# Kernel tuning notes

Hardware: AMD Instinct MI355X
Metric: run time of the kernel (lower is better)

## Reference

```python
import jax, jax.numpy as jnp
import numpy as np

K = 4  # number of neighbors, per kNN-VC convention

def setup_inputs() -> dict:
    key = jax.random.key(0)
    k1, k2 = jax.random.split(key)
    source_feats = jax.random.normal(k1, (2048, 1024), dtype=jnp.float32)
    target_feats = jax.random.normal(k2, (50000, 1024), dtype=jnp.float32)
    return {"source_feats": source_feats, "target_feats": target_feats}

def reference(source_feats, target_feats):
    # cosine kNN matching: for each source frame, find K nearest target frames
    # under cosine distance (= highest cosine similarity), then average them.
    eps = jnp.asarray(1e-8, source_feats.dtype)
    src_n = source_feats / jnp.maximum(jnp.linalg.norm(source_feats, axis=-1, keepdims=True), eps)
    tgt_n = target_feats / jnp.maximum(jnp.linalg.norm(target_feats, axis=-1, keepdims=True), eps)
    # [T_src, T_tgt] cosine similarity
    sims = jnp.einsum('sd,td->st', src_n, tgt_n)
    _, idx = jax.lax.top_k(sims, K)          # [T_src, K]
    neighbors = target_feats[idx]             # [T_src, K, D]
    out = jnp.mean(neighbors, axis=1)         # [T_src, D]
    return out
```

## Files before the change

### kernel.cpp

```cpp
#include <hip/hip_runtime.h>
#include <math.h>

#define S_ROWS 2048
#define T_ROWS 50000
#define DIM    1024
#define KNN    4

#define BM 128
#define BN 128
#define KSL 64
#define NSLAB (DIM / KSL)
#define NBUF 3
#define TILES_PER_CHUNK 2
#define CHUNK_COLS (BN * TILES_PER_CHUNK)
#define NUM_CHUNKS ((T_ROWS + CHUNK_COLS - 1) / CHUNK_COLS)
#define T_PAD (NUM_CHUNKS * CHUNK_COLS)
#define NCAND (NUM_CHUNKS * KNN)
#define REFINE 16
#define SP 67
#define QSCALE 500.0f

typedef unsigned int uint;
typedef unsigned long long u64;
typedef signed char i8;
typedef __attribute__((ext_vector_type(4))) int i32x4;

__device__ __forceinline__ u64 packI(int v, int idx) {
  return ((u64)((uint)v ^ 0x80000000u) << 32) | (uint)(~idx);
}

template <int N>
__device__ __forceinline__ void insU(u64 p, u64 (&tv)[N]) {
  if (p <= tv[N - 1]) return;
  tv[N - 1] = p;
#pragma unroll
  for (int j = N - 1; j > 0; --j) {
    if (tv[j] > tv[j - 1]) { u64 t = tv[j]; tv[j] = tv[j - 1]; tv[j - 1] = t; }
  }
}

__device__ __forceinline__ void llds16(const void* g, void* l) {
  __builtin_amdgcn_global_load_lds(
      reinterpret_cast<__attribute__((address_space(1))) void*>(
          reinterpret_cast<uintptr_t>(g)),
      reinterpret_cast<__attribute__((address_space(3))) void*>(
          (unsigned)reinterpret_cast<uintptr_t>(l)),
      16, 0, 0);
}

__device__ __forceinline__ int imax2(int a, int b) { return a > b ? a : b; }

__global__ __launch_bounds__(256) void quant2_kernel(const float* __restrict__ srcf,
                                                     const float* __restrict__ tgtf,
                                                     i8* __restrict__ srcq,
                                                     i8* __restrict__ tgtq) {
  const int b = blockIdx.x;
  const int tid = threadIdx.x;
  const bool isT = b < T_PAD;
  const int row = isT ? b : b - T_PAD;
  const float* in = isT ? tgtf : srcf;
  i8* outq = isT ? tgtq : srcq;
  const int nvalid = isT ? T_ROWS : S_ROWS;
  if (row >= nvalid) {
    ((uint*)(outq + ((size_t)row << 10)))[tid] = 0u;
    return;
  }
  __shared__ float red[4];
  float4 v = ((const float4*)(in + ((size_t)row << 10)))[tid];
  float s = v.x * v.x + v.y * v.y + v.z * v.z + v.w * v.w;
#pragma unroll
  for (int off = 32; off; off >>= 1) s += __shfl_down(s, off, 64);
  if ((tid & 63) == 0) red[tid >> 6] = s;
  __syncthreads();
  float tot = red[0] + red[1] + red[2] + red[3];
  float r = QSCALE / fmaxf(sqrtf(tot), 1e-8f);
  int q0 = __float2int_rn(v.x * r), q1 = __float2int_rn(v.y * r);
  int q2 = __float2int_rn(v.z * r), q3 = __float2int_rn(v.w * r);
  q0 = imax2(-127, (q0 < 127 ? q0 : 127));
  q1 = imax2(-127, (q1 < 127 ? q1 : 127));
  q2 = imax2(-127, (q2 < 127 ? q2 : 127));
  q3 = imax2(-127, (q3 < 127 ? q3 : 127));
  uint packed = ((uint)q0 & 255u) | (((uint)q1 & 255u) << 8) |
                (((uint)q2 & 255u) << 16) | (((uint)q3 & 255u) << 24);
  ((uint*)(outq + ((size_t)row << 10)))[tid] = packed;
}

union __align__(16) SimSmem {
  i8 ab[NBUF][2 * BM * KSL];
  int sims[BM * SP];
  u64 mb[256 * KNN];
};

__device__ __forceinline__ void stage64(const i8* aP, const i8* bP, i8* aL, i8* bL) {
  llds16(aP, aL);
  llds16(aP + 16384, aL + 1024);
  llds16(bP, bL);
  llds16(bP + 16384, bL + 1024);
}

__global__ __launch_bounds__(256, 3) void sim_i8_kernel(const i8* __restrict__ srcq,
                                                        const i8* __restrict__ tgtq,
                                                        u64* __restrict__ partials) {
  __shared__ SimSmem sm;

  const int tid = threadIdx.x;
  const int lane = tid & 63;
  const int wave = tid >> 6;
  const int qr = (wave >> 1) * 64;
  const int qch = wave & 1;
  const int m = lane & 15;
  const int quad = lane >> 4;
  const int r0 = blockIdx.x * BM;
  const int chunk = blockIdx.y;

  const int srow4 = lane >> 2;
  const int scb4 = (lane & 3) ^ (srow4 & 3);
  const i8* aLane = srcq + (((size_t)(r0 + wave * 32 + srow4)) << 10) + scb4 * 16;

  const int swz = (quad ^ (m & 3)) << 4;
  const int aoff0 = ((qr + m) << 6) + swz;
  const int boff0 = ((qch * 64 + m) << 6) + swz;

  u64 topp[KNN] = {0, 0, 0, 0};
  int thrI = (int)0x80000000;

  for (int tile = 0; tile < TILES_PER_CHUNK; ++tile) {
    const int c0 = chunk * CHUNK_COLS + tile * BN;
    const i8* bLane = tgtq + (((size_t)(c0 + wave * 32 + srow4)) << 10) + scb4 * 16;

    i32x4 acc[4][4];
#pragma unroll
    for (int i = 0; i < 4; ++i)
#pragma unroll
      for (int j = 0; j < 4; ++j) acc[i][j] = (i32x4){0, 0, 0, 0};

    stage64(aLane, bLane, sm.ab[0] + wave * 2048, sm.ab[0] + 8192 + wave * 2048);
    stage64(aLane + 64, bLane + 64, sm.ab[1] + wave * 2048, sm.ab[1] + 8192 + wave * 2048);

#pragma unroll
    for (int k = 0; k < NSLAB; ++k) {
      if (k == NSLAB - 1)
        asm volatile("s_waitcnt vmcnt(0)" ::: "memory");
      else
        asm volatile("s_waitcnt vmcnt(4)" ::: "memory");
      asm volatile("s_waitcnt lgkmcnt(0)" ::: "memory");
      __builtin_amdgcn_s_barrier();
      __builtin_amdgcn_sched_barrier(0);

      const i8* base = sm.ab[k % NBUF];
      i32x4 af[4], bf[4];
#pragma unroll
      for (int i = 0; i < 4; ++i) af[i] = *(const i32x4*)(base + aoff0 + i * 1024);
#pragma unroll
      for (int j = 0; j < 4; ++j) bf[j] = *(const i32x4*)(base + 8192 + boff0 + j * 1024);

      if (k + 2 < NSLAB) {
        i8* nb = sm.ab[(k + 2) % NBUF];
        stage64(aLane + ((k + 2) << 6), bLane + ((k + 2) << 6),
                nb + wave * 2048, nb + 8192 + wave * 2048);
      }

      __builtin_amdgcn_s_setprio(1);
#pragma unroll
      for (int i = 0; i < 4; ++i)
#pragma unroll
        for (int j = 0; j < 4; ++j)
          acc[i][j] = __builtin_amdgcn_mfma_i32_16x16x64_i8(af[i], bf[j], acc[i][j], 0, 0, 0);
      __builtin_amdgcn_s_setprio(0);
    }

    __syncthreads();

#pragma unroll
    for (int ph = 0; ph < 2; ++ph) {
      if (qch == ph) {
#pragma unroll
        for (int i = 0; i < 4; ++i)
#pragma unroll
          for (int j = 0; j < 4; ++j)
#pragma unroll
            for (int reg = 0; reg < 4; ++reg)
              sm.sims[(qr + i * 16 + quad * 4 + reg) * SP + j * 16 + m] = acc[i][j][reg];
      }
      __syncthreads();
      {
        const int rowl = tid & 127;
        const int chh = tid >> 7;
        const int* srow = &sm.sims[rowl * SP + chh * 32];
        const int gbase = c0 + ph * 64 + chh * 32;
#pragma unroll
        for (int c = 0; c < 32; c += 4) {
          int a = srow[c], b = srow[c + 1], d2 = srow[c + 2], e = srow[c + 3];
          int mx = imax2(imax2(a, b), imax2(d2, e));
          if (mx > thrI) {
            const int g = gbase + c;
            if (g + 0 < T_ROWS) insU<KNN>(packI(a, g + 0), topp);
            if (g + 1 < T_ROWS) insU<KNN>(packI(b, g + 1), topp);
            if (g + 2 < T_ROWS) insU<KNN>(packI(d2, g + 2), topp);
            if (g + 3 < T_ROWS) insU<KNN>(packI(e, g + 3), topp);
            thrI = (int)((uint)(topp[KNN - 1] >> 32) ^ 0x80000000u);
          }
        }
      }
      __syncthreads();
    }
  }

#pragma unroll
  for (int j = 0; j < KNN; ++j) sm.mb[tid * KNN + j] = topp[j];
  __syncthreads();
  if (tid < 128) {
#pragma unroll
    for (int j = 0; j < KNN; ++j) insU<KNN>(sm.mb[(tid + 128) * KNN + j], topp);
    u64* dst = partials + ((size_t)(r0 + tid) * NUM_CHUNKS + chunk) * KNN;
#pragma unroll
    for (int j = 0; j < KNN; ++j) dst[j] = topp[j];
  }
}

__global__ __launch_bounds__(256) void merge_gather_kernel(
    const u64* __restrict__ partials, const float* __restrict__ src,
    const float* __restrict__ tgt, float* __restrict__ out) {
  const int row = blockIdx.x;
  const int tid = threadIdx.x;
  const int lane = tid & 63;
  const int wave = tid >> 6;
  __shared__ u64 cbuf[NCAND];
  __shared__ u64 part8[8][REFINE];
  __shared__ int cand[REFINE];
  __shared__ double cval[REFINE];
  __shared__ int fin[KNN];

  for (int c = tid; c < NCAND; c += 256) cbuf[c] = partials[(size_t)row * NCAND + c];
  __syncthreads();

  if (tid < 8) {
    u64 t16[REFINE];
#pragma unroll
    for (int j = 0; j < REFINE; ++j) t16[j] = 0;
    const int base = tid * (NCAND / 8);
    for (int c = 0; c < NCAND / 8; ++c) insU<REFINE>(cbuf[base + c], t16);
#pragma unroll
    for (int j = 0; j < REFINE; ++j) part8[tid][j] = t16[j];
  }
  __syncthreads();
  if (tid == 0) {
    u64 t16[REFINE];
#pragma unroll
    for (int j = 0; j < REFINE; ++j) t16[j] = 0;
    for (int s = 0; s < 8; ++s)
#pragma unroll
      for (int j = 0; j < REFINE; ++j) insU<REFINE>(part8[s][j], t16);
#pragma unroll
    for (int j = 0; j < REFINE; ++j) cand[j] = (int)(~(uint)t16[j]);
  }
  __syncthreads();

  const float4* s4 = (const float4*)(src + ((size_t)row << 10));
  float4 s0 = s4[lane], s1 = s4[lane + 64], s2 = s4[lane + 128], s3 = s4[lane + 192];
  double ss = (double)s0.x * s0.x + (double)s0.y * s0.y + (double)s0.z * s0.z + (double)s0.w * s0.w
            + (double)s1.x * s1.x + (double)s1.y * s1.y + (double)s1.z * s1.z + (double)s1.w * s1.w
            + (double)s2.x * s2.x + (double)s2.y * s2.y + (double)s2.z * s2.z + (double)s2.w * s2.w
            + (double)s3.x * s3.x + (double)s3.y * s3.y + (double)s3.z * s3.z + (double)s3.w * s3.w;
#pragma unroll
  for (int off = 32; off; off >>= 1) ss += __shfl_down(ss, off, 64);
  ss = __shfl(ss, 0, 64);
  const double sn = fmax(sqrt(ss), 1e-8);

  for (int cc = wave; cc < REFINE; cc += 4) {
    const float4* t4 = (const float4*)(tgt + ((size_t)cand[cc] << 10));
    float4 t0 = t4[lane], t1 = t4[lane + 64], t2 = t4[lane + 128], t3 = t4[lane + 192];
    double dd = (double)s0.x * t0.x + (double)s0.y * t0.y + (double)s0.z * t0.z + (double)s0.w * t0.w
              + (double)s1.x * t1.x + (double)s1.y * t1.y + (double)s1.z * t1.z + (double)s1.w * t1.w
              + (double)s2.x * t2.x + (double)s2.y * t2.y + (double)s2.z * t2.z + (double)s2.w * t2.w
              + (double)s3.x * t3.x + (double)s3.y * t3.y + (double)s3.z * t3.z + (double)s3.w * t3.w;
    double tt = (double)t0.x * t0.x + (double)t0.y * t0.y + (double)t0.z * t0.z + (double)t0.w * t0.w
              + (double)t1.x * t1.x + (double)t1.y * t1.y + (double)t1.z * t1.z + (double)t1.w * t1.w
              + (double)t2.x * t2.x + (double)t2.y * t2.y + (double)t2.z * t2.z + (double)t2.w * t2.w
              + (double)t3.x * t3.x + (double)t3.y * t3.y + (double)t3.z * t3.z + (double)t3.w * t3.w;
#pragma unroll
    for (int off = 32; off; off >>= 1) {
      dd += __shfl_down(dd, off, 64);
      tt += __shfl_down(tt, off, 64);
    }
    if (lane == 0) cval[cc] = dd / (sn * fmax(sqrt(tt), 1e-8));
  }
  __syncthreads();

  if (tid == 0) {
    bool used[REFINE];
#pragma unroll
    for (int j = 0; j < REFINE; ++j) used[j] = false;
    for (int k = 0; k < KNN; ++k) {
      int bj = -1; double bv = 0.0; int bidx = 0x7fffffff;
      for (int j = 0; j < REFINE; ++j) {
        if (used[j]) continue;
        if (bj < 0 || cval[j] > bv || (cval[j] == bv && cand[j] < bidx)) {
          bj = j; bv = cval[j]; bidx = cand[j];
        }
      }
      used[bj] = true;
      fin[k] = cand[bj];
    }
  }
  __syncthreads();

  const int d = tid * 4;
  float4 a = *(const float4*)(tgt + ((size_t)fin[0] << 10) + d);
  float4 b = *(const float4*)(tgt + ((size_t)fin[1] << 10) + d);
  float4 c = *(const float4*)(tgt + ((size_t)fin[2] << 10) + d);
  float4 e = *(const float4*)(tgt + ((size_t)fin[3] << 10) + d);
  float4 o;
  o.x = 0.25f * (a.x + b.x + c.x + e.x);
  o.y = 0.25f * (a.y + b.y + c.y + e.y);
  o.z = 0.25f * (a.z + b.z + c.z + e.z);
  o.w = 0.25f * (a.w + b.w + c.w + e.w);
  *(float4*)(out + ((size_t)row << 10) + d) = o;
}

extern "C" void kernel_launch(void* const* d_in, const int* in_sizes, int n_in,
                              void* d_out, int out_size, void* d_ws, size_t ws_size,
                              hipStream_t stream) {
  const float* src = (const float*)d_in[0];
  const float* tgt = (const float*)d_in[1];
  float* out = (float*)d_out;
  char* ws = (char*)d_ws;

  const size_t SRCQ_B = (size_t)S_ROWS << 10;
  const size_t TGTQ_B = (size_t)T_PAD << 10;

  i8* srcq = (i8*)ws;
  i8* tgtq = (i8*)(ws + SRCQ_B);
  u64* partials = (u64*)(ws + SRCQ_B + TGTQ_B);

  quant2_kernel<<<T_PAD + S_ROWS, 256, 0, stream>>>(src, tgt, srcq, tgtq);

  dim3 g3(S_ROWS / BM, NUM_CHUNKS);
  sim_i8_kernel<<<g3, 256, 0, stream>>>(srcq, tgtq, partials);

  merge_gather_kernel<<<S_ROWS, 256, 0, stream>>>(partials, src, tgt, out);
}
```

Baseline: 681.5 us.

## Restructure similarity kernel into single-wave 64x64 blocks without barriers

Replaces the 256-thread 128x128 block with a single-wavefront block covering 64 source rows and four 64-column tiles per chunk. Double buffering uses a two-stage LDS ring, and with only one wave per block all workgroup barriers and the cross-wave top-k merge are removed. Each lane owns one source row and does its top-4 selection directly. The cost is less data reuse per block, with each wave loading A and B tiles alone, and more blocks. Occupancy depends on how many 64-thread blocks fit per CU given the LDS use.

```diff
diff --git a/kernel.cpp b/kernel.cpp
--- a/kernel.cpp
+++ b/kernel.cpp
@@ -6,13 +6,13 @@
 #define DIM    1024
 #define KNN    4
 
-#define BM 128
-#define BN 128
+#define BM 64
+#define TN 64
+#define TILES 4
 #define KSL 64
 #define NSLAB (DIM / KSL)
-#define NBUF 3
-#define TILES_PER_CHUNK 2
-#define CHUNK_COLS (BN * TILES_PER_CHUNK)
+#define NBUF 2
+#define CHUNK_COLS (TN * TILES)
 #define NUM_CHUNKS ((T_ROWS + CHUNK_COLS - 1) / CHUNK_COLS)
 #define T_PAD (NUM_CHUNKS * CHUNK_COLS)
 #define NCAND (NUM_CHUNKS * KNN)
@@ -88,45 +88,46 @@
 union __align__(16) SimSmem {
   i8 ab[NBUF][2 * BM * KSL];
   int sims[BM * SP];
-  u64 mb[256 * KNN];
 };
 
-__device__ __forceinline__ void stage64(const i8* aP, const i8* bP, i8* aL, i8* bL) {
-  llds16(aP, aL);
-  llds16(aP + 16384, aL + 1024);
-  llds16(bP, bL);
-  llds16(bP + 16384, bL + 1024);
-}
-
-__global__ __launch_bounds__(256, 3) void sim_i8_kernel(const i8* __restrict__ srcq,
-                                                        const i8* __restrict__ tgtq,
-                                                        u64* __restrict__ partials) {
+__device__ __forceinline__ void stage8(const i8* aP, const i8* bP, i8* buf) {
+  llds16(aP, buf);
+  llds16(aP + 16384, buf + 1024);
+  llds16(aP + 32768, buf + 2048);
+  llds16(aP + 49152, buf + 3072);
+  llds16(bP, buf + 4096);
+  llds16(bP + 16384, buf + 5120);
+  llds16(bP + 32768, buf + 6144);
+  llds16(bP + 49152, buf + 7168);
+}
+
+__global__ __launch_bounds__(64, 2) void sim_i8_kernel(const i8* __restrict__ srcq,
+                                                       const i8* __restrict__ tgtq,
+                                                       u64* __restrict__ partials) {
   __shared__ SimSmem sm;
 
-  const int tid = threadIdx.x;
-  const int lane = tid & 63;
-  const int wave = tid >> 6;
-  const int qr = (wave >> 1) * 64;
-  const int qch = wave & 1;
+  const int lane = threadIdx.x;
   const int m = lane & 15;
   const int quad = lane >> 4;
   const int r0 = blockIdx.x * BM;
   const int chunk = blockIdx.y;
+  const int c0 = chunk * CHUNK_COLS;
 
   const int srow4 = lane >> 2;
   const int scb4 = (lane & 3) ^ (srow4 & 3);
-  const i8* aLane = srcq + (((size_t)(r0 + wave * 32 + srow4)) << 10) + scb4 * 16;
+  const i8* aLane = srcq + (((size_t)(r0 + srow4)) << 10) + scb4 * 16;
 
   const int swz = (quad ^ (m & 3)) << 4;
-  const int aoff0 = ((qr + m) << 6) + swz;
-  const int boff0 = ((qch * 64 + m) << 6) + swz;
+  const int aoff0 = (m << 6) + swz;
+  const int boff0 = 4096 + (m << 6) + swz;
 
   u64 topp[KNN] = {0, 0, 0, 0};
   int thrI = (int)0x80000000;
 
-  for (int tile = 0; tile < TILES_PER_CHUNK; ++tile) {
-    const int c0 = chunk * CHUNK_COLS + tile * BN;
-    const i8* bLane = tgtq + (((size_t)(c0 + wave * 32 + srow4)) << 10) + scb4 * 16;
+#pragma unroll 1
+  for (int tile = 0; tile < TILES; ++tile) {
+    const int ct = c0 + tile * TN;
+    const i8* bLane = tgtq + (((size_t)(ct + srow4)) << 10) + scb4 * 16;
 
     i32x4 acc[4][4];
 #pragma unroll
@@ -134,31 +135,29 @@
 #pragma unroll
       for (int j = 0; j < 4; ++j) acc[i][j] = (i32x4){0, 0, 0, 0};
 
-    stage64(aLane, bLane, sm.ab[0] + wave * 2048, sm.ab[0] + 8192 + wave * 2048);
-    stage64(aLane + 64, bLane + 64, sm.ab[1] + wave * 2048, sm.ab[1] + 8192 + wave * 2048);
+    asm volatile("s_waitcnt lgkmcnt(0)" ::: "memory");
+    stage8(aLane, bLane, sm.ab[0]);
+    stage8(aLane + 64, bLane + 64, sm.ab[1]);
 
 #pragma unroll
     for (int k = 0; k < NSLAB; ++k) {
       if (k == NSLAB - 1)
         asm volatile("s_waitcnt vmcnt(0)" ::: "memory");
       else
-        asm volatile("s_waitcnt vmcnt(4)" ::: "memory");
+        asm volatile("s_waitcnt vmcnt(8)" ::: "memory");
+      __builtin_amdgcn_sched_barrier(0);
+
+      const i8* base = sm.ab[k & 1];
+      i32x4 af[4], bf[4];
+#pragma unroll
+      for (int i = 0; i < 4; ++i) af[i] = *(const i32x4*)(base + aoff0 + i * 1024);
+#pragma unroll
+      for (int j = 0; j < 4; ++j) bf[j] = *(const i32x4*)(base + boff0 + j * 1024);
+
       asm volatile("s_waitcnt lgkmcnt(0)" ::: "memory");
-      __builtin_amdgcn_s_barrier();
       __builtin_amdgcn_sched_barrier(0);
-
-      const i8* base = sm.ab[k % NBUF];
-      i32x4 af[4], bf[4];
-#pragma unroll
-      for (int i = 0; i < 4; ++i) af[i] = *(const i32x4*)(base + aoff0 + i * 1024);
-#pragma unroll
-      for (int j = 0; j < 4; ++j) bf[j] = *(const i32x4*)(base + 8192 + boff0 + j * 1024);
-
-      if (k + 2 < NSLAB) {
-        i8* nb = sm.ab[(k + 2) % NBUF];
-        stage64(aLane + ((k + 2) << 6), bLane + ((k + 2) << 6),
-                nb + wave * 2048, nb + 8192 + wave * 2048);
-      }
+      if (k + 2 < NSLAB)
+        stage8(aLane + ((k + 2) << 6), bLane + ((k + 2) << 6), sm.ab[k & 1]);
 
       __builtin_amdgcn_s_setprio(1);
 #pragma unroll
@@ -169,53 +168,37 @@
       __builtin_amdgcn_s_setprio(0);
     }
 
-    __syncthreads();
-
-#pragma unroll
-    for (int ph = 0; ph < 2; ++ph) {
-      if (qch == ph) {
-#pragma unroll
-        for (int i = 0; i < 4; ++i)
-#pragma unroll
-          for (int j = 0; j < 4; ++j)
-#pragma unroll
-            for (int reg = 0; reg < 4; ++reg)
-              sm.sims[(qr + i * 16 + quad * 4 + reg) * SP + j * 16 + m] = acc[i][j][reg];
-      }
-      __syncthreads();
-      {
-        const int rowl = tid & 127;
-        const int chh = tid >> 7;
-        const int* srow = &sm.sims[rowl * SP + chh * 32];
-        const int gbase = c0 + ph * 64 + chh * 32;
-#pragma unroll
-        for (int c = 0; c < 32; c += 4) {
-          int a = srow[c], b = srow[c + 1], d2 = srow[c + 2], e = srow[c + 3];
-          int mx = imax2(imax2(a, b), imax2(d2, e));
-          if (mx > thrI) {
-            const int g = gbase + c;
-            if (g + 0 < T_ROWS) insU<KNN>(packI(a, g + 0), topp);
-            if (g + 1 < T_ROWS) insU<KNN>(packI(b, g + 1), topp);
-            if (g + 2 < T_ROWS) insU<KNN>(packI(d2, g + 2), topp);
-            if (g + 3 < T_ROWS) insU<KNN>(packI(e, g + 3), topp);
-            thrI = (int)((uint)(topp[KNN - 1] >> 32) ^ 0x80000000u);
-          }
+#pragma unroll
+    for (int i = 0; i < 4; ++i)
+#pragma unroll
+      for (int j = 0; j < 4; ++j)
+#pragma unroll
+        for (int reg = 0; reg < 4; ++reg)
+          sm.sims[(i * 16 + quad * 4 + reg) * SP + j * 16 + m] = acc[i][j][reg];
+    asm volatile("s_waitcnt lgkmcnt(0)" ::: "memory");
+    __builtin_amdgcn_sched_barrier(0);
+
+    {
+      const int* srow = &sm.sims[lane * SP];
+#pragma unroll
+      for (int c = 0; c < TN; c += 4) {
+        int a = srow[c], b = srow[c + 1], d2 = srow[c + 2], e = srow[c + 3];
+        int mx = imax2(imax2(a, b), imax2(d2, e));
+        if (mx > thrI) {
+          const int g = ct + c;
+          if (g + 0 < T_ROWS) insU<KNN>(packI(a, g + 0), topp);
+          if (g + 1 < T_ROWS) insU<KNN>(packI(b, g + 1), topp);
+          if (g + 2 < T_ROWS) insU<KNN>(packI(d2, g + 2), topp);
+          if (g + 3 < T_ROWS) insU<KNN>(packI(e, g + 3), topp);
+          thrI = (int)((uint)(topp[KNN - 1] >> 32) ^ 0x80000000u);
         }
       }
-      __syncthreads();
     }
   }
 
-#pragma unroll
-  for (int j = 0; j < KNN; ++j) sm.mb[tid * KNN + j] = topp[j];
-  __syncthreads();
-  if (tid < 128) {
-#pragma unroll
-    for (int j = 0; j < KNN; ++j) insU<KNN>(sm.mb[(tid + 128) * KNN + j], topp);
-    u64* dst = partials + ((size_t)(r0 + tid) * NUM_CHUNKS + chunk) * KNN;
-#pragma unroll
-    for (int j = 0; j < KNN; ++j) dst[j] = topp[j];
-  }
+  u64* dst = partials + ((size_t)(r0 + lane) * NUM_CHUNKS + chunk) * KNN;
+#pragma unroll
+  for (int j = 0; j < KNN; ++j) dst[j] = topp[j];
 }
 
 __global__ __launch_bounds__(256) void merge_gather_kernel(
@@ -336,7 +319,7 @@
   quant2_kernel<<<T_PAD + S_ROWS, 256, 0, stream>>>(src, tgt, srcq, tgtq);
 
   dim3 g3(S_ROWS / BM, NUM_CHUNKS);
-  sim_i8_kernel<<<g3, 256, 0, stream>>>(srcq, tgtq, partials);
+  sim_i8_kernel<<<g3, 64, 0, stream>>>(srcq, tgtq, partials);
 
   merge_gather_kernel<<<S_ROWS, 256, 0, stream>>>(partials, src, tgt, out);
 }
```

New measurement: 674.8 us. Within noise of the previous version (-1.0%).
